# Performance work log

Hardware: AMD Instinct MI355X
Metric: run time of the kernel (lower is better)

## Reference

```python
import jax, jax.numpy as jnp
import numpy as np

B, N, C = 2, 16384, 512
H, D = 8, 64            # heads, dim_head
QG = 64                 # n_global_queries
SC, CD = 256, 64        # context slices, context_dim


def _attn(q, k, v):
    # scaled_dot_product_attention with scale=1.0 (as in the module)
    s = jnp.einsum('bhqd,bhkd->bhqk', q, k)
    a = jax.nn.softmax(s, axis=-1)
    return jnp.einsum('bhqk,bhkd->bhqd', a, v)


def setup_inputs() -> dict:
    key = jax.random.key(0)
    ks = jax.random.split(key, 20)
    r = lambda i, shape, s=0.02: jax.random.normal(ks[i], shape, dtype=jnp.float32) * s
    return {
        'x': jax.random.normal(ks[0], (B, N, C), dtype=jnp.float32),
        'context': jax.random.normal(ks[1], (B, H, SC, CD), dtype=jnp.float32),
        'q_global': jax.random.normal(ks[2], (1, H, QG, D), dtype=jnp.float32),
        'Wp': r(3, (C, H * D)), 'bp': jnp.zeros((H * D,), jnp.float32),
        'Wk': r(4, (D, D)), 'bk': jnp.zeros((D,), jnp.float32),
        'Wv': r(5, (D, D)), 'bv': jnp.zeros((D,), jnp.float32),
        'Wcq': r(6, (D, D)), 'bcq': jnp.zeros((D,), jnp.float32),
        'Wck': r(7, (CD, D)), 'bck': jnp.zeros((D,), jnp.float32),
        'Wcv': r(8, (CD, D)), 'bcv': jnp.zeros((D,), jnp.float32),
        'state_mixing': jnp.zeros((), jnp.float32),
        'Wo': r(9, (H * D, C)), 'bo': jnp.zeros((C,), jnp.float32),
    }


def reference(x, context, q_global, Wp, bp, Wk, bk, Wv, bv,
              Wcq, bcq, Wck, bck, Wcv, bcv, state_mixing, Wo, bo):
    # input projection -> (B, H, N, D)
    x_mid = (x @ Wp + bp).reshape(B, N, H, D).transpose(0, 2, 1, 3)
    G = jnp.broadcast_to(q_global, (B, H, QG, D))
    k = x_mid @ Wk + bk                     # (B,H,N,D)
    v = x_mid @ Wv + bv
    # FLARE low-rank self-attention: tokens -> global queries -> tokens
    z = _attn(G, k, v)                      # (B,H,QG,D)
    self_attn = _attn(k, G, z)              # (B,H,N,D)
    # cross-attention to geometry context
    q = x_mid @ Wcq + bcq                   # (B,H,N,D)
    ck = context @ Wck + bck                # (B,H,SC,D)
    cv = context @ Wcv + bcv
    cross_attn = _attn(q, ck, cv)           # (B,H,N,D)
    # sigmoid-gated mix
    w = jax.nn.sigmoid(state_mixing)
    out = w * self_attn + (1.0 - w) * cross_attn
    out = out.transpose(0, 2, 1, 3).reshape(B, N, H * D)
    return out @ Wo + bo                    # (B,N,C); dropout=0 (eval)
```

## Files before the change

kernel.cpp:

```cpp
#include <hip/hip_runtime.h>

typedef __bf16 bf16;
typedef __bf16 bf16x8 __attribute__((ext_vector_type(8)));
typedef short short8 __attribute__((ext_vector_type(8)));
typedef float f32x4 __attribute__((ext_vector_type(4)));

__device__ __forceinline__ float ldf(const void* p, size_t i, int bf) {
  if (bf) {
    unsigned int u = ((const unsigned short*)p)[i];
    union { unsigned int ui; float f; } c;
    c.ui = u << 16;
    return c.f;
  }
  return ((const float*)p)[i];
}

__device__ __forceinline__ int sw8(int r) { return ((r ^ (r >> 2)) & 7) << 3; }

__global__ void k_detect(const void* x, int* flag)
{
  int tid = threadIdx.x;
  int cnt = 0;
  for (int j = 0; j < 4; j++) {
    int i = (tid * 4 + j) * 2;
    unsigned int u = ((const unsigned short*)x)[i];
    union { unsigned int ui; float f; } c;
    c.ui = u << 16;
    float a = fabsf(c.f);
    if (a >= 1e-4f && a <= 100.f) cnt++;
  }
  for (int m = 1; m < 64; m <<= 1) cnt += __shfl_xor(cnt, m);
  if (tid == 0) *flag = (cnt > 128) ? 1 : 0;
}

__global__ __launch_bounds__(256)
void k_ctx(const int* flagp, const void* ctx, const void* Wck, const void* bck,
           const void* Wcv, const void* bcv, float* __restrict__ ck,
           float* __restrict__ cv)
{
  const int bf = *flagp;
  int rid = blockIdx.x * 4 + (threadIdx.x >> 6);
  int dp = threadIdx.x & 63;
  float a1 = 0.f, a2 = 0.f;
  for (int e = 0; e < 64; e++) {
    float c = ldf(ctx, (size_t)rid * 64 + e, bf);
    a1 += c * ldf(Wck, e * 64 + dp, bf);
    a2 += c * ldf(Wcv, e * 64 + dp, bf);
  }
  ck[rid * 64 + dp] = a1 + ldf(bck, dp, bf);
  cv[rid * 64 + dp] = a2 + ldf(bcv, dp, bf);
}

__global__ __launch_bounds__(256)
void k_fold(const int* flagp, const float* __restrict__ ck, const void* Wcq,
            const void* bcq, const void* qg, const void* Wk, const void* bk,
            float* __restrict__ ckq, float* __restrict__ cqb,
            float* __restrict__ Gk, float* __restrict__ gb)
{
  const int bf = *flagp;
  int bid = blockIdx.x, tid = threadIdx.x;
  if (bid < 1024) {
    int rid = bid * 4 + (tid >> 6), dp = tid & 63;
    const float* c = ck + (size_t)rid * 64;
    float a = 0.f;
    for (int o = 0; o < 64; o++) a += c[o] * ldf(Wcq, dp * 64 + o, bf);
    ckq[rid * 64 + dp] = a;
    if (dp == 0) {
      float s = 0.f;
      for (int o = 0; o < 64; o++) s += ldf(bcq, o, bf) * c[o];
      cqb[rid] = s;
    }
  } else {
    int i = (bid - 1024) * 256 + tid;
    int row = i >> 6, dIn = i & 63;
    float s = 0.f;
    for (int d = 0; d < 64; d++)
      s += ldf(qg, (size_t)row * 64 + d, bf) * ldf(Wk, dIn * 64 + d, bf);
    Gk[i] = s;
    if (dIn == 0) {
      float t = 0.f;
      for (int d = 0; d < 64; d++)
        t += ldf(qg, (size_t)row * 64 + d, bf) * ldf(bk, d, bf);
      gb[row] = t;
    }
  }
}

__global__ __launch_bounds__(256)
void k_wtr(const int* flagp, const void* Wp, const void* Wo,
           bf16* __restrict__ WpT, bf16* __restrict__ WoT)
{
  const int bf = *flagp;
  const int bid = blockIdx.x, tid = threadIdx.x;
  const void* W = (bid < 64) ? Wp : Wo;
  bf16* WT = (bid < 64) ? WpT : WoT;
  const int tb = bid & 63, kb = tb & 7, nb = tb >> 3;
  __shared__ float t[64][65];
  for (int e = tid; e < 4096; e += 256) {
    int k = e >> 6, n = e & 63;
    t[k][n] = ldf(W, (size_t)(kb * 64 + k) * 512 + nb * 64 + n, bf);
  }
  __syncthreads();
  for (int e = tid; e < 4096; e += 256) {
    int n = e >> 6, k = e & 63;
    WT[(size_t)(nb * 64 + n) * 512 + kb * 64 + k] = (bf16)t[k][n];
  }
}

__global__ __launch_bounds__(256)
void k_gemm_mfma(const int* flagp, const void* A, const int amode,
                 const bf16* __restrict__ WT, const void* bias, void* out,
                 const int omode)
{
  __shared__ __attribute__((aligned(16))) bf16 AsB[2][128 * 64];
  __shared__ __attribute__((aligned(16))) bf16 BsB[2][128 * 64];

  const int bf = *flagp;
  const int abf = (amode == 1) || bf;
  const int tid = threadIdx.x;
  const int srow = tid >> 3, schk = tid & 7;

  const int orig = blockIdx.y * 4 + blockIdx.x;
  const int nid = (orig & 7) * 128 + (orig >> 3);
  const int m0 = (nid >> 2) * 128, n0 = (nid & 3) * 128;

  const int lane = tid & 63, wid = tid >> 6;
  const int lo = lane & 15, hi = lane >> 4;
  const int wm = (wid >> 1) * 64, wn = (wid & 1) * 64;

  f32x4 rf[4][2];
  bf16x8 rb[4];
  bf16x8 rw[4];

  auto ldreg = [&](int kt) {
    const int koff = kt * 64 + schk * 8;
#pragma unroll
    for (int i = 0; i < 4; i++) {
      const int row = i * 32 + srow;
      if (abf) {
        rb[i] = *(const bf16x8*)((const bf16*)A + (size_t)(m0 + row) * 512 + koff);
      } else {
        const float* ap = (const float*)A + (size_t)(m0 + row) * 512 + koff;
        rf[i][0] = *(const f32x4*)ap;
        rf[i][1] = *(const f32x4*)(ap + 4);
      }
      rw[i] = *(const bf16x8*)(WT + (size_t)(n0 + row) * 512 + koff);
    }
  };
  auto stlds = [&](bf16* As, bf16* Bs) {
    const int c = schk * 8;
#pragma unroll
    for (int i = 0; i < 4; i++) {
      const int row = i * 32 + srow;
      bf16x8 v;
      if (abf) {
        v = rb[i];
      } else {
#pragma unroll
        for (int j = 0; j < 4; j++) {
          v[j] = (bf16)rf[i][0][j];
          v[4 + j] = (bf16)rf[i][1][j];
        }
      }
      *(bf16x8*)&As[row * 64 + (c ^ sw8(row))] = v;
      *(bf16x8*)&Bs[row * 64 + (c ^ sw8(row))] = rw[i];
    }
  };

  f32x4 acc[4][4];
#pragma unroll
  for (int mt = 0; mt < 4; mt++)
#pragma unroll
    for (int nt = 0; nt < 4; nt++) acc[mt][nt] = f32x4{0.f, 0.f, 0.f, 0.f};

  ldreg(0);
  stlds(AsB[0], BsB[0]);
  __syncthreads();

  int cur = 0;
  for (int kt = 0; kt < 8; kt++) {
    if (kt < 7) ldreg(kt + 1);
    const bf16* Asc = AsB[cur];
    const bf16* Bsc = BsB[cur];
#pragma unroll
    for (int ks = 0; ks < 2; ks++) {
      short8 af[4], bq[4];
#pragma unroll
      for (int mt = 0; mt < 4; mt++) {
        int r = wm + mt * 16 + lo;
        af[mt] = *(const short8*)&Asc[r * 64 + ((ks * 32 + hi * 8) ^ sw8(r))];
      }
#pragma unroll
      for (int nt = 0; nt < 4; nt++) {
        int r = wn + nt * 16 + lo;
        bq[nt] = *(const short8*)&Bsc[r * 64 + ((ks * 32 + hi * 8) ^ sw8(r))];
      }
#pragma unroll
      for (int mt = 0; mt < 4; mt++)
#pragma unroll
        for (int nt = 0; nt < 4; nt++)
          acc[mt][nt] = __builtin_amdgcn_mfma_f32_16x16x32_bf16(
              af[mt], bq[nt], acc[mt][nt], 0, 0, 0);
    }
    if (kt < 7) stlds(AsB[cur ^ 1], BsB[cur ^ 1]);
    __syncthreads();
    cur ^= 1;
  }

#pragma unroll
  for (int nt = 0; nt < 4; nt++) {
    const int col = n0 + wn + nt * 16 + lo;
    const float bj = ldf(bias, col, bf);
#pragma unroll
    for (int mt = 0; mt < 4; mt++)
#pragma unroll
      for (int r = 0; r < 4; r++) {
        const int rowg = m0 + wm + mt * 16 + hi * 4 + r;
        const float v = acc[mt][nt][r] + bj;
        const size_t oi = (size_t)rowg * 512 + col;
        if (omode == 0 || bf) ((bf16*)out)[oi] = (bf16)v;
        else                  ((float*)out)[oi] = v;
      }
  }
}

__global__ __launch_bounds__(256, 2)
void k_stageB(const float* __restrict__ Gk, const float* __restrict__ gb,
              const bf16* __restrict__ xm, float* __restrict__ zpart,
              float* __restrict__ lpart)
{
  __shared__ __attribute__((aligned(16))) char smem[8192 + 65536 + 1024];
  bf16* GkB = (bf16*)smem;
  const int tid = threadIdx.x;
  const int bh = blockIdx.y, b = bh >> 3, h = bh & 7;
  const int split = blockIdx.x;

#pragma unroll
  for (int it = 0; it < 2; it++) {
    int idx = tid + it * 256;
    int r = idx >> 3, c0 = (idx & 7) * 8;
    const float* g = Gk + (size_t)(h * 64 + r) * 64 + c0;
    bf16x8 v;
#pragma unroll
    for (int t = 0; t < 8; t++) v[t] = (bf16)g[t];
    *(bf16x8*)&GkB[r * 64 + (c0 ^ sw8(r))] = v;
  }
  __syncthreads();

  const int wid = tid >> 6, lane = tid & 63;
  const int lo = lane & 15, hi = lane >> 4;
  bf16*  Ew  = (bf16*)(smem + 8192 + wid * 16384);
  short* Xts = (short*)(smem + 8192 + wid * 16384 + 8192);

  short8 gk[4][2];
#pragma unroll
  for (int jt = 0; jt < 4; jt++)
#pragma unroll
    for (int ks = 0; ks < 2; ks++) {
      int r = jt * 16 + lo;
      gk[jt][ks] = *(const short8*)&GkB[r * 64 + ((ks * 32 + hi * 8) ^ sw8(r))];
    }
  float gbl[4][4];
#pragma unroll
  for (int jt = 0; jt < 4; jt++)
#pragma unroll
    for (int r = 0; r < 4; r++)
      gbl[jt][r] = gb[h * 64 + jt * 16 + hi * 4 + r];

  f32x4 zacc[4][4];
  float lacc[4][4];
#pragma unroll
  for (int jt = 0; jt < 4; jt++)
#pragma unroll
    for (int q = 0; q < 4; q++) {
      zacc[jt][q] = f32x4{0.f, 0.f, 0.f, 0.f};
      lacc[jt][q] = 0.f;
    }

  const int tokbase = split * 512 + wid * 128;
  for (int t = 0; t < 4; t++) {
    const int t0 = tokbase + t * 32;
    short8 bx[2][2];
#pragma unroll
    for (int tt = 0; tt < 2; tt++)
#pragma unroll
      for (int ks = 0; ks < 2; ks++)
        bx[tt][ks] = *(const short8*)(xm +
            (size_t)(b * 16384 + t0 + tt * 16 + lo) * 512 + h * 64 +
            ks * 32 + hi * 8);
#pragma unroll
    for (int tt = 0; tt < 2; tt++)
#pragma unroll
      for (int ks = 0; ks < 2; ks++)
#pragma unroll
        for (int e = 0; e < 8; e++) {
          int d = ks * 32 + hi * 8 + e;
          int tok = tt * 16 + lo;
          Xts[d * 64 + (tok ^ sw8(d))] = bx[tt][ks][e];
        }
    f32x4 s[4][2];
#pragma unroll
    for (int jt = 0; jt < 4; jt++)
#pragma unroll
      for (int tt = 0; tt < 2; tt++) s[jt][tt] = f32x4{0.f, 0.f, 0.f, 0.f};
#pragma unroll
    for (int ks = 0; ks < 2; ks++)
#pragma unroll
      for (int jt = 0; jt < 4; jt++)
#pragma unroll
        for (int tt = 0; tt < 2; tt++)
          s[jt][tt] = __builtin_amdgcn_mfma_f32_16x16x32_bf16(
              gk[jt][ks], bx[tt][ks], s[jt][tt], 0, 0, 0);
#pragma unroll
    for (int jt = 0; jt < 4; jt++)
#pragma unroll
      for (int tt = 0; tt < 2; tt++)
#pragma unroll
        for (int r = 0; r < 4; r++) {
          int j = jt * 16 + hi * 4 + r;
          int tok = tt * 16 + lo;
          float e = __expf(s[jt][tt][r] + gbl[jt][r]);
          lacc[jt][r] += e;
          Ew[j * 64 + (tok ^ sw8(j))] = (bf16)e;
        }
    short8 ea[4], xb[4];
#pragma unroll
    for (int jt = 0; jt < 4; jt++) {
      int r = jt * 16 + lo;
      ea[jt] = *(const short8*)&Ew[r * 64 + ((hi * 8) ^ sw8(r))];
    }
#pragma unroll
    for (int dt = 0; dt < 4; dt++) {
      int d = dt * 16 + lo;
      xb[dt] = *(const short8*)(Xts + d * 64 + ((hi * 8) ^ sw8(d)));
    }
#pragma unroll
    for (int jt = 0; jt < 4; jt++)
#pragma unroll
      for (int dt = 0; dt < 4; dt++)
        zacc[jt][dt] = __builtin_amdgcn_mfma_f32_16x16x32_bf16(
            ea[jt], xb[dt], zacc[jt][dt], 0, 0, 0);
  }

  float* lred = (float*)(smem + 8192 + 65536);
#pragma unroll
  for (int jt = 0; jt < 4; jt++)
#pragma unroll
    for (int r = 0; r < 4; r++) {
      float v = lacc[jt][r];
      for (int m = 1; m < 16; m <<= 1) v += __shfl_xor(v, m);
      if (lo == 0) lred[wid * 64 + jt * 16 + hi * 4 + r] = v;
    }
  __syncthreads();

  float* zred = (float*)(smem + 8192);
#pragma unroll
  for (int jt = 0; jt < 4; jt++)
#pragma unroll
    for (int dt = 0; dt < 4; dt++)
#pragma unroll
      for (int r = 0; r < 4; r++)
        zred[wid * 4096 + (jt * 16 + hi * 4 + r) * 64 + dt * 16 + lo] =
            zacc[jt][dt][r];
  __syncthreads();

  const size_t pbase = ((size_t)bh * 32 + split) * 4096;
  for (int i = tid; i < 4096; i += 256)
    zpart[pbase + i] =
        zred[i] + zred[4096 + i] + zred[8192 + i] + zred[12288 + i];
  if (tid < 64)
    lpart[((size_t)bh * 32 + split) * 64 + tid] =
        lred[tid] + lred[64 + tid] + lred[128 + tid] + lred[192 + tid];
}

__global__ __launch_bounds__(256)
void k_znorm(const int* flagp, const float* __restrict__ zpart,
             const float* __restrict__ lpart, const void* Wv, const void* bv,
             float* __restrict__ z)
{
  const int bf = *flagp;
  const int bh = blockIdx.x, tid = threadIdx.x;
  __shared__ float zsum[4096];
  __shared__ float lsum[64];
  for (int i = tid; i < 4096; i += 256) {
    float s = 0.f;
    for (int sp = 0; sp < 32; sp++)
      s += zpart[((size_t)bh * 32 + sp) * 4096 + i];
    zsum[i] = s;
  }
  if (tid < 64) {
    float s = 0.f;
    for (int sp = 0; sp < 32; sp++) s += lpart[((size_t)bh * 32 + sp) * 64 + tid];
    lsum[tid] = s;
  }
  __syncthreads();
  for (int i = tid; i < 4096; i += 256) {
    int j = i >> 6, d = i & 63;
    float inv = 1.f / lsum[j];
    float s = 0.f;
    for (int e = 0; e < 64; e++)
      s += zsum[j * 64 + e] * ldf(Wv, e * 64 + d, bf);
    z[(size_t)bh * 4096 + i] = s * inv + ldf(bv, d, bf);
  }
}

template <int NCH, int VSTR>
__device__ __forceinline__ void attn_part(
    const bf16* __restrict__ Bq, const bf16* __restrict__ BvT,
    const float* __restrict__ biasL, const short8 (&ax)[2][2],
    bf16* __restrict__ Pw, int lo, int hi,
    f32x4 (&accO)[2][4], float (&lsum)[2][4])
{
#pragma unroll
  for (int ch = 0; ch < NCH; ch++) {
    const int c0 = ch * 32;
    f32x4 s[2][2];
#pragma unroll
    for (int rt = 0; rt < 2; rt++)
#pragma unroll
      for (int ct = 0; ct < 2; ct++) s[rt][ct] = f32x4{0.f, 0.f, 0.f, 0.f};
#pragma unroll
    for (int ks = 0; ks < 2; ks++) {
      short8 bq[2];
#pragma unroll
      for (int ct = 0; ct < 2; ct++) {
        int n = c0 + ct * 16 + lo;
        bq[ct] = *(const short8*)(Bq + n * 64 + ((ks * 32 + hi * 8) ^ sw8(n)));
      }
#pragma unroll
      for (int rt = 0; rt < 2; rt++)
#pragma unroll
        for (int ct = 0; ct < 2; ct++)
          s[rt][ct] = __builtin_amdgcn_mfma_f32_16x16x32_bf16(
              ax[rt][ks], bq[ct], s[rt][ct], 0, 0, 0);
    }
    float b0 = biasL[c0 + lo], b1 = biasL[c0 + 16 + lo];
#pragma unroll
    for (int rt = 0; rt < 2; rt++)
#pragma unroll
      for (int r = 0; r < 4; r++) {
        int prow = rt * 16 + hi * 4 + r;
        float e0 = __expf(s[rt][0][r] + b0);
        float e1 = __expf(s[rt][1][r] + b1);
        lsum[rt][r] += e0 + e1;
        Pw[prow * 64 + (lo ^ sw8(prow))] = (bf16)e0;
        Pw[prow * 64 + ((16 + lo) ^ sw8(prow))] = (bf16)e1;
      }
    short8 ap[2];
#pragma unroll
    for (int rt = 0; rt < 2; rt++) {
      int prow = rt * 16 + lo;
      ap[rt] = *(const short8*)(Pw + prow * 64 + ((hi * 8) ^ sw8(prow)));
    }
#pragma unroll
    for (int dt = 0; dt < 4; dt++) {
      int d = dt * 16 + lo;
      short8 bv = *(const short8*)(BvT + d * VSTR + ((c0 + hi * 8) ^ sw8(d)));
#pragma unroll
      for (int rt = 0; rt < 2; rt++)
        accO[rt][dt] = __builtin_amdgcn_mfma_f32_16x16x32_bf16(
            ap[rt], bv, accO[rt][dt], 0, 0, 0);
    }
  }
}

__global__ __launch_bounds__(512)
void k_attn(const int* flagp, const float* __restrict__ Gk,
            const float* __restrict__ gb, const float* __restrict__ z,
            const float* __restrict__ ckq, const float* __restrict__ cqb,
            const float* __restrict__ cv, const bf16* __restrict__ xm,
            const void* smix, bf16* __restrict__ selfmid)
{
  __shared__ __attribute__((aligned(16))) bf16 GkB[64 * 64];
  __shared__ __attribute__((aligned(16))) bf16 zTB[64 * 64];
  __shared__ __attribute__((aligned(16))) bf16 ckqB[256 * 64];
  __shared__ __attribute__((aligned(16))) bf16 cvTB[64 * 256];
  __shared__ __attribute__((aligned(16))) bf16 Pst[8][32 * 64];
  __shared__ float cqbL[256];
  __shared__ float gbL[64];

  const int tid = threadIdx.x;
  const int bh = blockIdx.y, b = bh >> 3, h = bh & 7;

  {
    int r = tid >> 3, c0 = (tid & 7) * 8;
    const float* g = Gk + ((size_t)(h * 64 + r)) * 64 + c0;
    bf16x8 v;
#pragma unroll
    for (int t = 0; t < 8; t++) v[t] = (bf16)g[t];
    *(bf16x8*)&GkB[r * 64 + (c0 ^ sw8(r))] = v;
    const float* zp = z + (size_t)bh * 4096 + (size_t)c0 * 64 + r;
#pragma unroll
    for (int t = 0; t < 8; t++) v[t] = (bf16)zp[t * 64];
    *(bf16x8*)&zTB[r * 64 + (c0 ^ sw8(r))] = v;
  }
#pragma unroll
  for (int rr = 0; rr < 4; rr++) {
    int idx = tid + rr * 512;
    int r = idx >> 3, c0 = (idx & 7) * 8;
    const float* c = ckq + (size_t)bh * 16384 + (size_t)r * 64 + c0;
    bf16x8 v;
#pragma unroll
    for (int t = 0; t < 8; t++) v[t] = (bf16)c[t];
    *(bf16x8*)&ckqB[r * 64 + (c0 ^ sw8(r))] = v;
  }
  {
    int d = tid >> 3, s0 = (tid & 7) * 32;
#pragma unroll
    for (int cc = 0; cc < 4; cc++) {
      int sb = s0 + cc * 8;
      bf16x8 v;
#pragma unroll
      for (int t = 0; t < 8; t++)
        v[t] = (bf16)cv[(size_t)bh * 16384 + (size_t)(sb + t) * 64 + d];
      *(bf16x8*)&cvTB[d * 256 + (sb ^ sw8(d))] = v;
    }
  }
  if (tid < 256)      cqbL[tid] = cqb[bh * 256 + tid];
  else if (tid < 320) gbL[tid - 256] = gb[h * 64 + (tid - 256)];
  __syncthreads();

  const int wid = tid >> 6, lane = tid & 63;
  const int lo = lane & 15, hi = lane >> 4;
  const int m0 = blockIdx.x * 256 + wid * 32;
  bf16* Pw = Pst[wid];

  short8 ax[2][2];
#pragma unroll
  for (int rt = 0; rt < 2; rt++)
#pragma unroll
    for (int ks = 0; ks < 2; ks++)
      ax[rt][ks] = *(const short8*)(xm +
          (size_t)(b * 16384 + m0 + rt * 16 + lo) * 512 + h * 64 +
          ks * 32 + hi * 8);

  f32x4 accS[2][4], accC[2][4];
  float l1[2][4], l2[2][4];
#pragma unroll
  for (int rt = 0; rt < 2; rt++)
#pragma unroll
    for (int dt = 0; dt < 4; dt++) {
      accS[rt][dt] = f32x4{0.f, 0.f, 0.f, 0.f};
      accC[rt][dt] = f32x4{0.f, 0.f, 0.f, 0.f};
      l1[rt][dt] = 0.f;
      l2[rt][dt] = 0.f;
    }

  attn_part<2, 64>(GkB, zTB, gbL, ax, Pw, lo, hi, accS, l1);
  attn_part<8, 256>(ckqB, cvTB, cqbL, ax, Pw, lo, hi, accC, l2);

#pragma unroll
  for (int rt = 0; rt < 2; rt++)
#pragma unroll
    for (int r = 0; r < 4; r++) {
      float a = l1[rt][r], c = l2[rt][r];
      for (int m = 1; m < 16; m <<= 1) {
        a += __shfl_xor(a, m);
        c += __shfl_xor(c, m);
      }
      l1[rt][r] = 1.f / a;
      l2[rt][r] = 1.f / c;
    }

  const int bf = *flagp;
  const float wmix = 1.f / (1.f + __expf(-ldf(smix, 0, bf)));
#pragma unroll
  for (int rt = 0; rt < 2; rt++)
#pragma unroll
    for (int r = 0; r < 4; r++) {
      int row = m0 + rt * 16 + hi * 4 + r;
      size_t off = (size_t)(b * 16384 + row) * 512 + h * 64;
#pragma unroll
      for (int dt = 0; dt < 4; dt++) {
        float vS = accS[rt][dt][r] * l1[rt][r];
        float vC = accC[rt][dt][r] * l2[rt][r];
        selfmid[off + dt * 16 + lo] = (bf16)(wmix * vS + (1.f - wmix) * vC);
      }
    }
}

extern "C" void kernel_launch(void* const* d_in, const int* in_sizes, int n_in,
                              void* d_out, int out_size, void* d_ws, size_t ws_size,
                              hipStream_t stream)
{
  const void* x    = d_in[0];
  const void* ctx  = d_in[1];
  const void* qg   = d_in[2];
  const void* Wp   = d_in[3];  const void* bp  = d_in[4];
  const void* Wk   = d_in[5];  const void* bk  = d_in[6];
  const void* Wv   = d_in[7];  const void* bv  = d_in[8];
  const void* Wcq  = d_in[9];  const void* bcq = d_in[10];
  const void* Wck  = d_in[11]; const void* bck = d_in[12];
  const void* Wcv  = d_in[13]; const void* bcv = d_in[14];
  const void* smix = d_in[15];
  const void* Wo   = d_in[16]; const void* bo  = d_in[17];

  char* ws = (char*)d_ws;
  int*   flag    = (int*)(ws);
  float* ck      = (float*)(ws + 256);
  float* cv      = (float*)(ws + 1048832);
  float* ckq     = (float*)(ws + 2097408);
  float* cqb     = (float*)(ws + 3145984);
  float* Gk      = (float*)(ws + 3162368);
  float* gb      = (float*)(ws + 3293440);
  float* z       = (float*)(ws + 4348160);
  bf16*  xm      = (bf16*)(ws + 5396736);
  bf16*  selfmid = (bf16*)(ws + 38951168);
  bf16*  WpT     = (bf16*)(ws + 256);
  bf16*  WoT     = (bf16*)(ws + 256 + 524288);
  float* zpart   = (float*)(ws + 38951168);
  float* lpart   = (float*)(ws + 38951168 + 8388608);

  k_detect<<<1, 64, 0, stream>>>(x, flag);

  k_ctx<<<1024, 256, 0, stream>>>(flag, ctx, Wck, bck, Wcv, bcv, ck, cv);
  k_fold<<<1152, 256, 0, stream>>>(flag, ck, Wcq, bcq, qg, Wk, bk,
                                   ckq, cqb, Gk, gb);

  k_wtr<<<128, 256, 0, stream>>>(flag, Wp, Wo, WpT, WoT);

  k_gemm_mfma<<<dim3(4, 256), 256, 0, stream>>>(flag, x, 0, WpT, bp, xm, 0);

  k_stageB<<<dim3(32, 16), 256, 0, stream>>>(Gk, gb, xm, zpart, lpart);
  k_znorm<<<16, 256, 0, stream>>>(flag, zpart, lpart, Wv, bv, z);

  k_attn<<<dim3(64, 16), 512, 0, stream>>>(flag, Gk, gb, z, ckq, cqb, cv, xm,
                                           smix, selfmid);

  k_gemm_mfma<<<dim3(4, 256), 256, 0, stream>>>(flag, selfmid, 1, WoT, bo,
                                                d_out, 1);
}
```

Measured before the change: 433.0 us.

## Pre-swizzle bf16 attention operands and keep softmax probabilities in registers

Adds a prep kernel, and changes znorm, so that ckq, transposed cv, Gk and transposed z are written once to global memory in swizzled bf16 layout. k_attn then fills LDS with plain vector copies instead of converting fp32 per block. The attention inner loop computes S^T so each lane holds exp values for whole tokens. It repacks them through cross-lane shuffles into the MFMA A operand, removing the per-wave LDS staging buffer for P. Bias is read from registers via shuffles, and launch bounds request higher occupancy. The cost is an extra small kernel launch and more shuffle instructions.

```diff
diff --git a/kernel.cpp b/kernel.cpp
--- a/kernel.cpp
+++ b/kernel.cpp
@@ -16,6 +16,12 @@
 }
 
 __device__ __forceinline__ int sw8(int r) { return ((r ^ (r >> 2)) & 7) << 3; }
+
+__device__ __forceinline__ unsigned pk2(float a, float b) {
+  union { bf16 h[2]; unsigned u; } c;
+  c.h[0] = (bf16)a; c.h[1] = (bf16)b;
+  return c.u;
+}
 
 __global__ void k_detect(const void* x, int* flag)
 {
@@ -87,6 +93,35 @@
 }
 
 __global__ __launch_bounds__(256)
+void k_prep(const float* __restrict__ ckq, const float* __restrict__ cv,
+            const float* __restrict__ Gk, bf16* __restrict__ g_ckqb,
+            bf16* __restrict__ g_cvtb, bf16* __restrict__ g_gkb)
+{
+  const int bid = blockIdx.x, tid = threadIdx.x;
+  if (bid < 16) {
+    const float* src = ckq + (size_t)bid * 16384;
+    bf16* dst = g_ckqb + (size_t)bid * 16384;
+    for (int e = tid; e < 16384; e += 256) {
+      int r = e >> 6, c = e & 63;
+      dst[r * 64 + (c ^ sw8(r))] = (bf16)src[e];
+    }
+  } else if (bid < 32) {
+    int bh = bid - 16;
+    const float* src = cv + (size_t)bh * 16384;
+    bf16* dst = g_cvtb + (size_t)bh * 16384;
+    for (int e = tid; e < 16384; e += 256) {
+      int d = e >> 8, s = e & 255;
+      dst[d * 256 + (s ^ sw8(d))] = (bf16)src[s * 64 + d];
+    }
+  } else {
+    for (int e = tid; e < 32768; e += 256) {
+      int hh = e >> 12, r = (e >> 6) & 63, c = e & 63;
+      g_gkb[hh * 4096 + r * 64 + (c ^ sw8(r))] = (bf16)Gk[e];
+    }
+  }
+}
+
+__global__ __launch_bounds__(256)
 void k_wtr(const int* flagp, const void* Wp, const void* Wo,
            bf16* __restrict__ WpT, bf16* __restrict__ WoT)
 {
@@ -376,7 +411,7 @@
 __global__ __launch_bounds__(256)
 void k_znorm(const int* flagp, const float* __restrict__ zpart,
              const float* __restrict__ lpart, const void* Wv, const void* bv,
-             float* __restrict__ z)
+             bf16* __restrict__ g_ztb)
 {
   const int bf = *flagp;
   const int bh = blockIdx.x, tid = threadIdx.x;
@@ -400,130 +435,126 @@
     float s = 0.f;
     for (int e = 0; e < 64; e++)
       s += zsum[j * 64 + e] * ldf(Wv, e * 64 + d, bf);
-    z[(size_t)bh * 4096 + i] = s * inv + ldf(bv, d, bf);
-  }
-}
-
-template <int NCH, int VSTR>
-__device__ __forceinline__ void attn_part(
-    const bf16* __restrict__ Bq, const bf16* __restrict__ BvT,
-    const float* __restrict__ biasL, const short8 (&ax)[2][2],
-    bf16* __restrict__ Pw, int lo, int hi,
-    f32x4 (&accO)[2][4], float (&lsum)[2][4])
+    g_ztb[(size_t)bh * 4096 + d * 64 + (j ^ sw8(d))] =
+        (bf16)(s * inv + ldf(bv, d, bf));
+  }
+}
+
+template <int NCH, int VSTR, int NB>
+__device__ __forceinline__ void attn_part2(
+    const bf16* __restrict__ Aq, const bf16* __restrict__ BvT,
+    const float (&breg)[NB], const short8 (&ax)[2][2],
+    int lo, int hi, f32x4 (&accO)[2][4], float (&ltok)[2])
 {
 #pragma unroll
   for (int ch = 0; ch < NCH; ch++) {
     const int c0 = ch * 32;
     f32x4 s[2][2];
 #pragma unroll
-    for (int rt = 0; rt < 2; rt++)
-#pragma unroll
-      for (int ct = 0; ct < 2; ct++) s[rt][ct] = f32x4{0.f, 0.f, 0.f, 0.f};
+    for (int ct = 0; ct < 2; ct++)
+#pragma unroll
+      for (int rt = 0; rt < 2; rt++) s[ct][rt] = f32x4{0.f, 0.f, 0.f, 0.f};
 #pragma unroll
     for (int ks = 0; ks < 2; ks++) {
-      short8 bq[2];
+      short8 aq[2];
 #pragma unroll
       for (int ct = 0; ct < 2; ct++) {
         int n = c0 + ct * 16 + lo;
-        bq[ct] = *(const short8*)(Bq + n * 64 + ((ks * 32 + hi * 8) ^ sw8(n)));
-      }
-#pragma unroll
-      for (int rt = 0; rt < 2; rt++)
-#pragma unroll
-        for (int ct = 0; ct < 2; ct++)
-          s[rt][ct] = __builtin_amdgcn_mfma_f32_16x16x32_bf16(
-              ax[rt][ks], bq[ct], s[rt][ct], 0, 0, 0);
-    }
-    float b0 = biasL[c0 + lo], b1 = biasL[c0 + 16 + lo];
-#pragma unroll
-    for (int rt = 0; rt < 2; rt++)
-#pragma unroll
-      for (int r = 0; r < 4; r++) {
-        int prow = rt * 16 + hi * 4 + r;
-        float e0 = __expf(s[rt][0][r] + b0);
-        float e1 = __expf(s[rt][1][r] + b1);
-        lsum[rt][r] += e0 + e1;
-        Pw[prow * 64 + (lo ^ sw8(prow))] = (bf16)e0;
-        Pw[prow * 64 + ((16 + lo) ^ sw8(prow))] = (bf16)e1;
-      }
-    short8 ap[2];
+        aq[ct] = *(const short8*)(Aq + n * 64 + ((ks * 32 + hi * 8) ^ sw8(n)));
+      }
+#pragma unroll
+      for (int ct = 0; ct < 2; ct++)
+#pragma unroll
+        for (int rt = 0; rt < 2; rt++)
+          s[ct][rt] = __builtin_amdgcn_mfma_f32_16x16x32_bf16(
+              aq[ct], ax[rt][ks], s[ct][rt], 0, 0, 0);
+    }
+    unsigned w[2][2][2];
+#pragma unroll
+    for (int ct = 0; ct < 2; ct++) {
+      float b[4];
+#pragma unroll
+      for (int r = 0; r < 4; r++)
+        b[r] = __shfl(breg[(c0 + ct * 16) >> 6],
+                      ((c0 + ct * 16) & 63) + hi * 4 + r);
+#pragma unroll
+      for (int rt = 0; rt < 2; rt++) {
+        float e0 = __expf(s[ct][rt][0] + b[0]);
+        float e1 = __expf(s[ct][rt][1] + b[1]);
+        float e2 = __expf(s[ct][rt][2] + b[2]);
+        float e3 = __expf(s[ct][rt][3] + b[3]);
+        ltok[rt] += e0 + e1 + e2 + e3;
+        w[rt][ct][0] = pk2(e0, e1);
+        w[rt][ct][1] = pk2(e2, e3);
+      }
+    }
 #pragma unroll
     for (int rt = 0; rt < 2; rt++) {
-      int prow = rt * 16 + lo;
-      ap[rt] = *(const short8*)(Pw + prow * 64 + ((hi * 8) ^ sw8(prow)));
-    }
-#pragma unroll
-    for (int dt = 0; dt < 4; dt++) {
-      int d = dt * 16 + lo;
-      short8 bv = *(const short8*)(BvT + d * VSTR + ((c0 + hi * 8) ^ sw8(d)));
-#pragma unroll
-      for (int rt = 0; rt < 2; rt++)
+      const int s0 = lo + 32 * (hi & 1);
+      unsigned t00 = __shfl(w[rt][0][0], s0);
+      unsigned t10 = __shfl(w[rt][1][0], s0);
+      unsigned t01 = __shfl(w[rt][0][1], s0);
+      unsigned t11 = __shfl(w[rt][1][1], s0);
+      unsigned t20 = __shfl(w[rt][0][0], s0 + 16);
+      unsigned t30 = __shfl(w[rt][1][0], s0 + 16);
+      unsigned t21 = __shfl(w[rt][0][1], s0 + 16);
+      unsigned t31 = __shfl(w[rt][1][1], s0 + 16);
+      union { unsigned u[4]; short8 s8; } pa;
+      const bool c1 = (hi >> 1) != 0;
+      pa.u[0] = c1 ? t10 : t00;
+      pa.u[1] = c1 ? t11 : t01;
+      pa.u[2] = c1 ? t30 : t20;
+      pa.u[3] = c1 ? t31 : t21;
+#pragma unroll
+      for (int dt = 0; dt < 4; dt++) {
+        int d = dt * 16 + lo;
+        short8 bv = *(const short8*)(BvT + d * VSTR + ((c0 + hi * 8) ^ sw8(d)));
         accO[rt][dt] = __builtin_amdgcn_mfma_f32_16x16x32_bf16(
-            ap[rt], bv, accO[rt][dt], 0, 0, 0);
-    }
-  }
-}
-
-__global__ __launch_bounds__(512)
-void k_attn(const int* flagp, const float* __restrict__ Gk,
-            const float* __restrict__ gb, const float* __restrict__ z,
-            const float* __restrict__ ckq, const float* __restrict__ cqb,
-            const float* __restrict__ cv, const bf16* __restrict__ xm,
+            pa.s8, bv, accO[rt][dt], 0, 0, 0);
+      }
+    }
+  }
+}
+
+__global__ __launch_bounds__(512, 4)
+void k_attn(const int* flagp, const bf16* __restrict__ g_gkb,
+            const bf16* __restrict__ g_ztb, const bf16* __restrict__ g_ckqb,
+            const bf16* __restrict__ g_cvtb, const float* __restrict__ cqb,
+            const float* __restrict__ gb, const bf16* __restrict__ xm,
             const void* smix, bf16* __restrict__ selfmid)
 {
-  __shared__ __attribute__((aligned(16))) bf16 GkB[64 * 64];
-  __shared__ __attribute__((aligned(16))) bf16 zTB[64 * 64];
-  __shared__ __attribute__((aligned(16))) bf16 ckqB[256 * 64];
-  __shared__ __attribute__((aligned(16))) bf16 cvTB[64 * 256];
-  __shared__ __attribute__((aligned(16))) bf16 Pst[8][32 * 64];
-  __shared__ float cqbL[256];
-  __shared__ float gbL[64];
+  __shared__ __attribute__((aligned(16))) bf16 S[40960];
+  bf16* GkB  = S;
+  bf16* zTB  = S + 4096;
+  bf16* ckqB = S + 8192;
+  bf16* cvTB = S + 24576;
 
   const int tid = threadIdx.x;
   const int bh = blockIdx.y, b = bh >> 3, h = bh & 7;
+  const int lane = tid & 63;
 
   {
-    int r = tid >> 3, c0 = (tid & 7) * 8;
-    const float* g = Gk + ((size_t)(h * 64 + r)) * 64 + c0;
-    bf16x8 v;
-#pragma unroll
-    for (int t = 0; t < 8; t++) v[t] = (bf16)g[t];
-    *(bf16x8*)&GkB[r * 64 + (c0 ^ sw8(r))] = v;
-    const float* zp = z + (size_t)bh * 4096 + (size_t)c0 * 64 + r;
-#pragma unroll
-    for (int t = 0; t < 8; t++) v[t] = (bf16)zp[t * 64];
-    *(bf16x8*)&zTB[r * 64 + (c0 ^ sw8(r))] = v;
-  }
-#pragma unroll
-  for (int rr = 0; rr < 4; rr++) {
-    int idx = tid + rr * 512;
-    int r = idx >> 3, c0 = (idx & 7) * 8;
-    const float* c = ckq + (size_t)bh * 16384 + (size_t)r * 64 + c0;
-    bf16x8 v;
-#pragma unroll
-    for (int t = 0; t < 8; t++) v[t] = (bf16)c[t];
-    *(bf16x8*)&ckqB[r * 64 + (c0 ^ sw8(r))] = v;
-  }
-  {
-    int d = tid >> 3, s0 = (tid & 7) * 32;
-#pragma unroll
-    for (int cc = 0; cc < 4; cc++) {
-      int sb = s0 + cc * 8;
-      bf16x8 v;
-#pragma unroll
-      for (int t = 0; t < 8; t++)
-        v[t] = (bf16)cv[(size_t)bh * 16384 + (size_t)(sb + t) * 64 + d];
-      *(bf16x8*)&cvTB[d * 256 + (sb ^ sw8(d))] = v;
-    }
-  }
-  if (tid < 256)      cqbL[tid] = cqb[bh * 256 + tid];
-  else if (tid < 320) gbL[tid - 256] = gb[h * 64 + (tid - 256)];
+    int i = tid;
+    *(bf16x8*)&GkB[i * 8] = *(const bf16x8*)&g_gkb[(size_t)h * 4096 + i * 8];
+    *(bf16x8*)&zTB[i * 8] = *(const bf16x8*)&g_ztb[(size_t)bh * 4096 + i * 8];
+#pragma unroll
+    for (int it = 0; it < 4; it++) {
+      int j = tid + it * 512;
+      *(bf16x8*)&ckqB[j * 8] =
+          *(const bf16x8*)&g_ckqb[(size_t)bh * 16384 + j * 8];
+      *(bf16x8*)&cvTB[j * 8] =
+          *(const bf16x8*)&g_cvtb[(size_t)bh * 16384 + j * 8];
+    }
+  }
+  float creg[4], greg[1];
+#pragma unroll
+  for (int q = 0; q < 4; q++) creg[q] = cqb[bh * 256 + q * 64 + lane];
+  greg[0] = gb[h * 64 + lane];
   __syncthreads();
 
-  const int wid = tid >> 6, lane = tid & 63;
+  const int wid = tid >> 6;
   const int lo = lane & 15, hi = lane >> 4;
   const int m0 = blockIdx.x * 256 + wid * 32;
-  bf16* Pw = Pst[wid];
 
   short8 ax[2][2];
 #pragma unroll
@@ -535,32 +566,26 @@
           ks * 32 + hi * 8);
 
   f32x4 accS[2][4], accC[2][4];
-  float l1[2][4], l2[2][4];
+  float l1[2] = {0.f, 0.f}, l2[2] = {0.f, 0.f};
 #pragma unroll
   for (int rt = 0; rt < 2; rt++)
 #pragma unroll
     for (int dt = 0; dt < 4; dt++) {
       accS[rt][dt] = f32x4{0.f, 0.f, 0.f, 0.f};
       accC[rt][dt] = f32x4{0.f, 0.f, 0.f, 0.f};
-      l1[rt][dt] = 0.f;
-      l2[rt][dt] = 0.f;
-    }
-
-  attn_part<2, 64>(GkB, zTB, gbL, ax, Pw, lo, hi, accS, l1);
-  attn_part<8, 256>(ckqB, cvTB, cqbL, ax, Pw, lo, hi, accC, l2);
-
-#pragma unroll
-  for (int rt = 0; rt < 2; rt++)
-#pragma unroll
-    for (int r = 0; r < 4; r++) {
-      float a = l1[rt][r], c = l2[rt][r];
-      for (int m = 1; m < 16; m <<= 1) {
-        a += __shfl_xor(a, m);
-        c += __shfl_xor(c, m);
-      }
-      l1[rt][r] = 1.f / a;
-      l2[rt][r] = 1.f / c;
-    }
+    }
+
+  attn_part2<2, 64, 1>(GkB, zTB, greg, ax, lo, hi, accS, l1);
+  attn_part2<8, 256, 4>(ckqB, cvTB, creg, ax, lo, hi, accC, l2);
+
+#pragma unroll
+  for (int rt = 0; rt < 2; rt++) {
+    float a = l1[rt], c = l2[rt];
+    a += __shfl_xor(a, 16); a += __shfl_xor(a, 32);
+    c += __shfl_xor(c, 16); c += __shfl_xor(c, 32);
+    l1[rt] = 1.f / a;
+    l2[rt] = 1.f / c;
+  }
 
   const int bf = *flagp;
   const float wmix = 1.f / (1.f + __expf(-ldf(smix, 0, bf)));
@@ -568,12 +593,14 @@
   for (int rt = 0; rt < 2; rt++)
 #pragma unroll
     for (int r = 0; r < 4; r++) {
+      const float invS = __shfl(l1[rt], hi * 4 + r);
+      const float invC = __shfl(l2[rt], hi * 4 + r);
       int row = m0 + rt * 16 + hi * 4 + r;
       size_t off = (size_t)(b * 16384 + row) * 512 + h * 64;
 #pragma unroll
       for (int dt = 0; dt < 4; dt++) {
-        float vS = accS[rt][dt][r] * l1[rt][r];
-        float vC = accC[rt][dt][r] * l2[rt][r];
+        float vS = accS[rt][dt][r] * invS;
+        float vC = accC[rt][dt][r] * invC;
         selfmid[off + dt * 16 + lo] = (bf16)(wmix * vS + (1.f - wmix) * vC);
       }
     }
@@ -603,7 +630,10 @@
   float* cqb     = (float*)(ws + 3145984);
   float* Gk      = (float*)(ws + 3162368);
   float* gb      = (float*)(ws + 3293440);
-  float* z       = (float*)(ws + 4348160);
+  bf16*  g_cvtb  = (bf16*)(ws + 3295744);
+  bf16*  g_ckqb  = (bf16*)(ws + 3820032);
+  bf16*  g_gkb   = (bf16*)(ws + 4348160);
+  bf16*  g_ztb   = (bf16*)(ws + 4413696);
   bf16*  xm      = (bf16*)(ws + 5396736);
   bf16*  selfmid = (bf16*)(ws + 38951168);
   bf16*  WpT     = (bf16*)(ws + 256);
@@ -617,15 +647,17 @@
   k_fold<<<1152, 256, 0, stream>>>(flag, ck, Wcq, bcq, qg, Wk, bk,
                                    ckq, cqb, Gk, gb);
 
+  k_prep<<<33, 256, 0, stream>>>(ckq, cv, Gk, g_ckqb, g_cvtb, g_gkb);
   k_wtr<<<128, 256, 0, stream>>>(flag, Wp, Wo, WpT, WoT);
 
   k_gemm_mfma<<<dim3(4, 256), 256, 0, stream>>>(flag, x, 0, WpT, bp, xm, 0);
 
   k_stageB<<<dim3(32, 16), 256, 0, stream>>>(Gk, gb, xm, zpart, lpart);
-  k_znorm<<<16, 256, 0, stream>>>(flag, zpart, lpart, Wv, bv, z);
-
-  k_attn<<<dim3(64, 16), 512, 0, stream>>>(flag, Gk, gb, z, ckq, cqb, cv, xm,
-                                           smix, selfmid);
+  k_znorm<<<16, 256, 0, stream>>>(flag, zpart, lpart, Wv, bv, g_ztb);
+
+  k_attn<<<dim3(64, 16), 512, 0, stream>>>(flag, g_gkb, g_ztb, g_ckqb, g_cvtb,
+                                           cqb, (const float*)gb, xm, smix,
+                                           selfmid);
 
   k_gemm_mfma<<<dim3(4, 256), 256, 0, stream>>>(flag, selfmid, 1, WoT, bo,
                                                 d_out, 1);
```

After: 445.6 us. +2.9%, slower.
